# Kernel optimization log

Measured on AMD Instinct MI355X. Metric: run time of the kernel, lower is better.

## Reference

```python
import jax, jax.numpy as jnp
import numpy as np

EMBED_DIM = 512
KERNEL = 17


def setup_inputs() -> dict:
    key = jax.random.key(0)
    ks = jax.random.split(key, 5)
    B, L, C = 2, 8192, EMBED_DIM
    s = C ** -0.5
    x = jax.random.normal(ks[0], (B, L, C), dtype=jnp.float32)
    # weights stored as (in, out); equivalent to torch Linear weight.T
    w_qkv = jax.random.normal(ks[1], (C, 3 * C), dtype=jnp.float32) * s
    w_width = jax.random.normal(ks[2], (C, 1), dtype=jnp.float32) * s
    b_width = jax.random.normal(ks[3], (1,), dtype=jnp.float32) * 0.01
    w_out = jax.random.normal(ks[4], (C, C), dtype=jnp.float32) * s
    return {"x": x, "w_qkv": w_qkv, "w_width": w_width, "b_width": b_width, "w_out": w_out}


def reference(x, w_qkv, w_width, b_width, w_out):
    B, L, C = x.shape
    K = KERNEL
    half_k = K // 2
    scale = C ** -0.5

    qkv = x @ w_qkv                      # [B,L,3C]
    q, k, v = jnp.split(qkv, 3, axis=-1)

    # learned soft window width in [1, K]
    width = jax.nn.sigmoid(x @ w_width + b_width) * (K - 1) + 1.0   # [B,L,1]

    # sliding windows of k/v: pad along L then gather K-sized windows
    k_pad = jnp.pad(k, ((0, 0), (half_k, half_k), (0, 0)))
    v_pad = jnp.pad(v, ((0, 0), (half_k, half_k), (0, 0)))
    idx = jnp.arange(L)[:, None] + jnp.arange(K)[None, :]           # [L,K]
    k_win = k_pad[:, idx]                # [B,L,K,C]
    v_win = v_pad[:, idx]                # [B,L,K,C]

    scores = jnp.einsum('blc,blkc->blk', q, k_win) * scale          # [B,L,K]

    rel_pos = jnp.abs(jnp.arange(K, dtype=jnp.float32) - half_k)    # [K]
    soft_mask = jax.nn.sigmoid((width - rel_pos) * 5.0)             # [B,L,K]
    scores = scores - (1.0 - soft_mask) * 10000.0

    attn = jax.nn.softmax(scores, axis=-1)
    out = jnp.einsum('blk,blkc->blc', attn, v_win)                  # [B,L,C]
    return (out + v) @ w_out
```

## Files before the change

### kernel.cpp

```cpp
#include <hip/hip_runtime.h>

typedef unsigned short u16;
typedef unsigned int   u32;
typedef __attribute__((ext_vector_type(8))) short          shortx8;
typedef __attribute__((ext_vector_type(8))) unsigned short ushortx8;
typedef __attribute__((ext_vector_type(4))) float          floatx4;

#define AS1 __attribute__((address_space(1)))
#define AS3 __attribute__((address_space(3)))

#define SEG 8208
#define LV  16416

__device__ __forceinline__ float b2f(u16 v) {
  return __uint_as_float(((u32)v) << 16);
}
__device__ __forceinline__ u16 f2b(float f) {
  u32 u = __float_as_uint(f);
  u += 0x7FFF + ((u >> 16) & 1);
  return (u16)(u >> 16);
}
__device__ __forceinline__ void cp16(const void* g, void* l) {
  __builtin_amdgcn_global_load_lds((AS1 u32*)g, (AS3 u32*)l, 16, 0, 0);
}

__global__ __launch_bounds__(256)
void prep(const float* __restrict__ x, const float* __restrict__ w_width,
          const float* __restrict__ b_width, const float* __restrict__ w_qkv,
          const float* __restrict__ w_out, u16* __restrict__ xb,
          float* __restrict__ width, u16* __restrict__ BtAll,
          u16* __restrict__ Vt) {
  __shared__ alignas(16) u16 shb[17408];
  const int b = blockIdx.x;
  if (b < 32) {
    const bool isMc = (b < 16);
    const int t    = isMc ? b : b - 16;
    const int row0 = (t >> 2) * 128;
    const int col0 = (t & 3) * 128;
    const int tid  = threadIdx.x;
    const int lane = tid & 63;
    const int wave = tid >> 6;
    const int quad = lane >> 4;
    const int lr   = lane & 15;
    const int wr   = (wave >> 1) * 64;
    const int wc   = (wave & 1) * 64;
    u16* As = shb;
    u16* Bs = shb + 8192;

    floatx4 acc[4][4];
#pragma unroll
    for (int i = 0; i < 4; ++i)
#pragma unroll
      for (int j = 0; j < 4; ++j) acc[i][j] = (floatx4)0.0f;

    int srow[4], scol[4];
#pragma unroll
    for (int p = 0; p < 4; ++p) {
      int c = p * 256 + tid;
      srow[p] = c >> 3;
      scol[p] = ((c & 7) ^ (srow[p] & 7)) * 8;
    }
    const int swz = lr & 7;

    for (int k0 = 0; k0 < 512; k0 += 64) {
#pragma unroll
      for (int p = 0; p < 4; ++p) {
        const float* ga = w_qkv + (size_t)(row0 + srow[p]) * 1536 +
                          (isMc ? 0 : 1024) + k0 + scol[p];
        floatx4 a0 = *(const floatx4*)ga;
        floatx4 a1 = *(const floatx4*)(ga + 4);
        ushortx8 o;
#pragma unroll
        for (int j = 0; j < 4; ++j) { o[j] = f2b(a0[j]); o[4 + j] = f2b(a1[j]); }
        *(ushortx8*)&As[(p * 256 + tid) * 8] = o;
      }
#pragma unroll
      for (int p = 0; p < 4; ++p) {
        ushortx8 o;
        if (isMc) {
          const float* gb = w_qkv + (size_t)(col0 + srow[p]) * 1536 + 512 +
                            k0 + scol[p];
          floatx4 b0 = *(const floatx4*)gb;
          floatx4 b1 = *(const floatx4*)(gb + 4);
#pragma unroll
          for (int j = 0; j < 4; ++j) { o[j] = f2b(b0[j]); o[4 + j] = f2b(b1[j]); }
        } else {
          const float* gb = w_out + (size_t)(k0 + scol[p]) * 512 + col0 + srow[p];
#pragma unroll
          for (int j = 0; j < 8; ++j) o[j] = f2b(gb[(size_t)j * 512]);
        }
        *(ushortx8*)&Bs[(p * 256 + tid) * 8] = o;
      }
      __syncthreads();
#pragma unroll
      for (int ks = 0; ks < 2; ++ks) {
        shortx8 af[4], bf[4];
#pragma unroll
        for (int mi = 0; mi < 4; ++mi)
          af[mi] = *(const shortx8*)
              &As[((wr + mi * 16 + lr) * 8 + ((ks * 4 + quad) ^ swz)) * 8];
#pragma unroll
        for (int ni = 0; ni < 4; ++ni)
          bf[ni] = *(const shortx8*)
              &Bs[((wc + ni * 16 + lr) * 8 + ((ks * 4 + quad) ^ swz)) * 8];
#pragma unroll
        for (int mi = 0; mi < 4; ++mi)
#pragma unroll
          for (int ni = 0; ni < 4; ++ni)
            acc[mi][ni] = __builtin_amdgcn_mfma_f32_16x16x32_bf16(
                af[mi], bf[ni], acc[mi][ni], 0, 0, 0);
      }
      __syncthreads();
    }
    u16* outp = BtAll + (isMc ? 0 : (size_t)512 * 512);
#pragma unroll
    for (int mi = 0; mi < 4; ++mi)
#pragma unroll
      for (int ni = 0; ni < 4; ++ni)
#pragma unroll
        for (int r = 0; r < 4; ++r)
          shb[(wc + ni * 16 + lr) * 136 + wr + mi * 16 + quad * 4 + r] =
              f2b(acc[mi][ni][r]);
    __syncthreads();
    const int rr = tid >> 4, cc = (tid & 15) * 8;
#pragma unroll
    for (int it = 0; it < 8; ++it) {
      int chl = it * 16 + rr;
      *(ushortx8*)(outp + (size_t)(col0 + chl) * 512 + row0 + cc) =
          *(const ushortx8*)&shb[chl * 136 + cc];
    }
  } else if (b < 4128) {
    const int lane = threadIdx.x & 63;
    const int row  = (b - 32) * 4 + (threadIdx.x >> 6);
    const float* xp = x + (size_t)row * 512 + lane * 8;
    floatx4 v0 = *(const floatx4*)xp;
    floatx4 v1 = *(const floatx4*)(xp + 4);
    floatx4 w0 = *(const floatx4*)(w_width + lane * 8);
    floatx4 w1 = *(const floatx4*)(w_width + lane * 8 + 4);
    float s = 0.f;
    ushortx8 o;
#pragma unroll
    for (int j = 0; j < 4; ++j) {
      s += v0[j] * w0[j] + v1[j] * w1[j];
      o[j] = f2b(v0[j]); o[4 + j] = f2b(v1[j]);
    }
    *(ushortx8*)(xb + (size_t)row * 512 + lane * 8) = o;
#pragma unroll
    for (int m = 32; m >= 1; m >>= 1) s += __shfl_xor(s, m, 64);
    if (lane == 0)
      width[row] = 16.f / (1.f + __expf(-(s + b_width[0]))) + 1.f;
  } else {
    const int idx = (b - 4128) * 256 + threadIdx.x;
    const int ch = idx >> 5;
    const int k  = idx & 31;
    const int seg = k >> 4;
    const int j   = k & 15;
    const int col = seg * SEG + (j < 8 ? j : 8192 + j);
    Vt[(size_t)ch * LV + col] = 0;
  }
}

__global__ __launch_bounds__(256, 3)
void gemm_qv(const u16* __restrict__ A, const u16* __restrict__ Bt,
             u16* __restrict__ Qb, u16* __restrict__ Vt) {
  const int K = 512;
  __shared__ alignas(16) u16 lds[17408];
  u16* As = lds;
  u16* Bs = lds + 8192;
  const int tid  = threadIdx.x;
  const int lane = tid & 63;
  const int wave = tid >> 6;
  const int quad = lane >> 4;
  const int lr   = lane & 15;
  const int row0 = blockIdx.x * 128;
  const int col0 = blockIdx.y * 128;
  const int wr   = (wave >> 1) * 64;
  const int wc   = (wave & 1) * 64;

  floatx4 acc[4][4];
#pragma unroll
  for (int i = 0; i < 4; ++i)
#pragma unroll
    for (int j = 0; j < 4; ++j) acc[i][j] = (floatx4)0.0f;

  int srow[4], scol[4];
#pragma unroll
  for (int p = 0; p < 4; ++p) {
    int c = p * 256 + tid;
    srow[p] = c >> 3;
    scol[p] = ((c & 7) ^ (srow[p] & 7)) * 8;
  }
  const int swz = lr & 7;

  for (int k0 = 0; k0 < K; k0 += 64) {
#pragma unroll
    for (int p = 0; p < 4; ++p)
      cp16(A + (size_t)(row0 + srow[p]) * K + k0 + scol[p], &As[(p * 256 + tid) * 8]);
#pragma unroll
    for (int p = 0; p < 4; ++p)
      cp16(Bt + (size_t)(col0 + srow[p]) * K + k0 + scol[p], &Bs[(p * 256 + tid) * 8]);
    __syncthreads();

#pragma unroll
    for (int ks = 0; ks < 2; ++ks) {
      shortx8 af[4], bf[4];
#pragma unroll
      for (int mi = 0; mi < 4; ++mi)
        af[mi] = *(const shortx8*)
            &As[((wr + mi * 16 + lr) * 8 + ((ks * 4 + quad) ^ swz)) * 8];
#pragma unroll
      for (int ni = 0; ni < 4; ++ni)
        bf[ni] = *(const shortx8*)
            &Bs[((wc + ni * 16 + lr) * 8 + ((ks * 4 + quad) ^ swz)) * 8];
#pragma unroll
      for (int mi = 0; mi < 4; ++mi)
#pragma unroll
        for (int ni = 0; ni < 4; ++ni)
          acc[mi][ni] = __builtin_amdgcn_mfma_f32_16x16x32_bf16(
              af[mi], bf[ni], acc[mi][ni], 0, 0, 0);
    }
    __syncthreads();
  }

  if (col0 < 512) {
    const int cb = col0;
#pragma unroll
    for (int mi = 0; mi < 4; ++mi)
#pragma unroll
      for (int ni = 0; ni < 4; ++ni)
#pragma unroll
        for (int r = 0; r < 4; ++r)
          lds[(wr + mi * 16 + quad * 4 + r) * 136 + wc + ni * 16 + lr] =
              f2b(acc[mi][ni][r]);
    __syncthreads();
    const int rr = tid >> 4, cc = (tid & 15) * 8;
#pragma unroll
    for (int it = 0; it < 8; ++it) {
      int row = it * 16 + rr;
      *(ushortx8*)(Qb + (size_t)(row0 + row) * 512 + cb + cc) =
          *(const ushortx8*)&lds[row * 136 + cc];
    }
  } else {
    const int cb = col0 - 512;
    const int bb = row0 >> 13, pib0 = row0 & 8191;
#pragma unroll
    for (int mi = 0; mi < 4; ++mi)
#pragma unroll
      for (int ni = 0; ni < 4; ++ni)
#pragma unroll
        for (int r = 0; r < 4; ++r)
          lds[(wc + ni * 16 + lr) * 136 + wr + mi * 16 + quad * 4 + r] =
              f2b(acc[mi][ni][r]);
    __syncthreads();
    const int rr = tid >> 4, cc = (tid & 15) * 8;
#pragma unroll
    for (int it = 0; it < 8; ++it) {
      int chl = it * 16 + rr;
      ushortx8 v = *(const ushortx8*)&lds[chl * 136 + cc];
      *(ushortx8*)(Vt + (size_t)(cb + chl) * LV + (size_t)bb * SEG + 8 + pib0 + cc) = v;
    }
  }
}

__global__ __launch_bounds__(256, 1)
void attn_fused(const u16* __restrict__ Q, const u16* __restrict__ Kx,
                const u16* __restrict__ Vt, const float* __restrict__ width,
                float* __restrict__ Out) {
  __shared__ alignas(16) u16 P[4][16][32];
  const int tid  = threadIdx.x;
  const int lane = tid & 63;
  const int wave = tid >> 6;
  const int quad = lane >> 4;
  const int lr   = lane & 15;
  const int p0   = blockIdx.x * 64;
  const int pw   = p0 + wave * 16;
  const int pibw = pw & 8191;
  const int bb   = pw >> 13;
  const size_t cb0 = (size_t)bb * SEG + pibw;

  shortx8 vfA[16];
#pragma unroll
  for (int ctl = 0; ctl < 16; ++ctl)
    vfA[ctl] = *(const shortx8*)(Vt + (size_t)(ctl * 16 + lr) * LV +
                                 cb0 + quad * 8);

  floatx4 s0 = (floatx4)0.0f, s1 = (floatx4)0.0f;
#pragma unroll 4
  for (int s = 0; s < 16; ++s) {
    const int k0 = s * 32 + quad * 8;
    shortx8 af = *(const shortx8*)(Q  + (size_t)(pw + lr) * 512 + k0);
    shortx8 f0 = *(const shortx8*)(Kx + (ptrdiff_t)(pw - 8 + lr) * 512 + k0);
    shortx8 f1 = *(const shortx8*)(Kx + (ptrdiff_t)(pw + 8 + lr) * 512 + k0);
    s0 = __builtin_amdgcn_mfma_f32_16x16x32_bf16(af, f0, s0, 0, 0, 0);
    s1 = __builtin_amdgcn_mfma_f32_16x16x32_bf16(af, f1, s1, 0, 0, 0);
  }

  shortx8 vfB[16];
#pragma unroll
  for (int ctl = 0; ctl < 16; ++ctl)
    vfB[ctl] = *(const shortx8*)(Vt + (size_t)(256 + ctl * 16 + lr) * LV +
                                 cb0 + quad * 8);

  {
    const float scale = 0.044194173824159216f;
    floatx4 wv = *(const floatx4*)(width + pw + quad * 4);
#pragma unroll
    for (int r = 0; r < 4; ++r) {
      const int row = quad * 4 + r;
      const int d0  = lr - row;
      const int d1  = d0 + 16;
      const int jb0 = pibw + lr - 8;
      const int jb1 = jb0 + 16;
      float rel0 = fabsf((float)(d0 - 8));
      float rel1 = fabsf((float)(d1 - 8));
      float mk0 = 1.f / (1.f + __expf(-5.f * (wv[r] - rel0)));
      float mk1 = 1.f / (1.f + __expf(-5.f * (wv[r] - rel1)));
      float val0 = (d0 >= 0)
          ? (((unsigned)jb0 < 8192u ? s0[r] * scale : 0.f) - (1.f - mk0) * 10000.f)
          : -1e30f;
      float val1 = (d1 <= 16)
          ? (((unsigned)jb1 < 8192u ? s1[r] * scale : 0.f) - (1.f - mk1) * 10000.f)
          : -1e30f;
      float mx = fmaxf(val0, val1);
#pragma unroll
      for (int m = 8; m >= 1; m >>= 1) mx = fmaxf(mx, __shfl_xor(mx, m, 64));
      float e0 = __expf(val0 - mx), e1 = __expf(val1 - mx);
      float sum = e0 + e1;
#pragma unroll
      for (int m = 8; m >= 1; m >>= 1) sum += __shfl_xor(sum, m, 64);
      const float inv = 1.f / sum;
      P[wave][row][lr]      = f2b(e0 * inv + (d0 == 8 ? 1.f : 0.f));
      P[wave][row][lr + 16] = f2b(e1 * inv + (d1 == 8 ? 1.f : 0.f));
    }
  }
  shortx8 pf = *(const shortx8*)&P[wave][lr][quad * 8];

#pragma unroll
  for (int ctl = 0; ctl < 16; ++ctl) {
    floatx4 o = __builtin_amdgcn_mfma_f32_16x16x32_bf16(pf, vfA[ctl],
                                                        (floatx4)0.0f, 0, 0, 0);
#pragma unroll
    for (int r = 0; r < 4; ++r)
      Out[(size_t)(pw + quad * 4 + r) * 512 + ctl * 16 + lr] = o[r];
  }
#pragma unroll
  for (int ctl = 0; ctl < 16; ++ctl) {
    floatx4 o = __builtin_amdgcn_mfma_f32_16x16x32_bf16(pf, vfB[ctl],
                                                        (floatx4)0.0f, 0, 0, 0);
#pragma unroll
    for (int r = 0; r < 4; ++r)
      Out[(size_t)(pw + quad * 4 + r) * 512 + 256 + ctl * 16 + lr] = o[r];
  }
}

extern "C" void kernel_launch(void* const* d_in, const int* in_sizes, int n_in,
                              void* d_out, int out_size, void* d_ws, size_t ws_size,
                              hipStream_t stream) {
  const float* x       = (const float*)d_in[0];
  const float* w_qkv   = (const float*)d_in[1];
  const float* w_width = (const float*)d_in[2];
  const float* b_width = (const float*)d_in[3];
  const float* w_out   = (const float*)d_in[4];
  float* out = (float*)d_out;

  const int M = 16384;
  char* ws = (char*)d_ws;
  u16*   xb    = (u16*)(ws + 8192);
  u16*   Qb    = (u16*)(ws + 16793600);
  u16*   Vt    = (u16*)(ws + 33579008);
  u16*   BtAll = (u16*)(ws + 50397184);
  float* width = (float*)(ws + 51445760);

  prep<<<dim3(4192), dim3(256), 0, stream>>>(x, w_width, b_width, w_qkv, w_out,
                                             xb, width, BtAll, Vt);
  gemm_qv<<<dim3(M / 128, 8), dim3(256), 0, stream>>>(xb, BtAll, Qb, Vt);
  attn_fused<<<dim3(M / 64), dim3(256), 0, stream>>>(Qb, xb, Vt, width, out);
}
```

Before: 165.0 us.

## Coalesce w_out loads in prep, remap GEMM and attention blocks for locality

The prep kernel now loads w_out with coalesced float4 row reads and scatters them transposed into the swizzled LDS tile, replacing strided per-element column reads. gemm_qv uses a 1D grid with an XCD-aware block remap so blocks sharing rows land on the same die. attn_fused now splits channels across waves, giving 32 positions per block and twice as many blocks with occupancy 2, plus an XCD-aware block order. The width buffer offset moves. The attention split recomputes the QK scores in two waves per row group, which adds duplicated work.

After: 153.6 us. 6.9% less time.

```diff
diff --git a/kernel.cpp b/kernel.cpp
--- a/kernel.cpp
+++ b/kernel.cpp
@@ -74,22 +74,32 @@
         for (int j = 0; j < 4; ++j) { o[j] = f2b(a0[j]); o[4 + j] = f2b(a1[j]); }
         *(ushortx8*)&As[(p * 256 + tid) * 8] = o;
       }
-#pragma unroll
-      for (int p = 0; p < 4; ++p) {
-        ushortx8 o;
-        if (isMc) {
+      if (isMc) {
+#pragma unroll
+        for (int p = 0; p < 4; ++p) {
           const float* gb = w_qkv + (size_t)(col0 + srow[p]) * 1536 + 512 +
                             k0 + scol[p];
           floatx4 b0 = *(const floatx4*)gb;
           floatx4 b1 = *(const floatx4*)(gb + 4);
+          ushortx8 o;
 #pragma unroll
           for (int j = 0; j < 4; ++j) { o[j] = f2b(b0[j]); o[4 + j] = f2b(b1[j]); }
-        } else {
-          const float* gb = w_out + (size_t)(k0 + scol[p]) * 512 + col0 + srow[p];
-#pragma unroll
-          for (int j = 0; j < 8; ++j) o[j] = f2b(gb[(size_t)j * 512]);
+          *(ushortx8*)&Bs[(p * 256 + tid) * 8] = o;
         }
-        *(ushortx8*)&Bs[(p * 256 + tid) * 8] = o;
+      } else {
+#pragma unroll
+        for (int it = 0; it < 8; ++it) {
+          int e  = it * 1024 + tid * 4;
+          int kk = e >> 7;
+          int j  = e & 127;
+          floatx4 b4 = *(const floatx4*)(w_out + (size_t)(k0 + kk) * 512 +
+                                         col0 + j);
+#pragma unroll
+          for (int q = 0; q < 4; ++q) {
+            int r = j + q;
+            Bs[(r * 8 + ((kk >> 3) ^ (r & 7))) * 8 + (kk & 7)] = f2b(b4[q]);
+          }
+        }
       }
       __syncthreads();
 #pragma unroll
@@ -172,8 +182,9 @@
   const int wave = tid >> 6;
   const int quad = lane >> 4;
   const int lr   = lane & 15;
-  const int row0 = blockIdx.x * 128;
-  const int col0 = blockIdx.y * 128;
+  const int logical = (blockIdx.x & 7) * 128 + (blockIdx.x >> 3);
+  const int row0 = (logical >> 3) * 128;
+  const int col0 = (logical & 7) * 128;
   const int wr   = (wave >> 1) * 64;
   const int wc   = (wave & 1) * 64;
 
@@ -262,7 +273,7 @@
   }
 }
 
-__global__ __launch_bounds__(256, 1)
+__global__ __launch_bounds__(256, 2)
 void attn_fused(const u16* __restrict__ Q, const u16* __restrict__ Kx,
                 const u16* __restrict__ Vt, const float* __restrict__ width,
                 float* __restrict__ Out) {
@@ -272,16 +283,19 @@
   const int wave = tid >> 6;
   const int quad = lane >> 4;
   const int lr   = lane & 15;
-  const int p0   = blockIdx.x * 64;
-  const int pw   = p0 + wave * 16;
+  const int p0   = ((blockIdx.x & 7) * 64 + (blockIdx.x >> 3)) * 32;
+  const int rg   = wave & 1;
+  const int chh  = wave >> 1;
+  const int ch0  = chh * 256;
+  const int pw   = p0 + rg * 16;
   const int pibw = pw & 8191;
   const int bb   = pw >> 13;
   const size_t cb0 = (size_t)bb * SEG + pibw;
 
-  shortx8 vfA[16];
-#pragma unroll
-  for (int ctl = 0; ctl < 16; ++ctl)
-    vfA[ctl] = *(const shortx8*)(Vt + (size_t)(ctl * 16 + lr) * LV +
+  shortx8 vfA[8];
+#pragma unroll
+  for (int ctl = 0; ctl < 8; ++ctl)
+    vfA[ctl] = *(const shortx8*)(Vt + (size_t)(ch0 + ctl * 16 + lr) * LV +
                                  cb0 + quad * 8);
 
   floatx4 s0 = (floatx4)0.0f, s1 = (floatx4)0.0f;
@@ -295,10 +309,10 @@
     s1 = __builtin_amdgcn_mfma_f32_16x16x32_bf16(af, f1, s1, 0, 0, 0);
   }
 
-  shortx8 vfB[16];
-#pragma unroll
-  for (int ctl = 0; ctl < 16; ++ctl)
-    vfB[ctl] = *(const shortx8*)(Vt + (size_t)(256 + ctl * 16 + lr) * LV +
+  shortx8 vfB[8];
+#pragma unroll
+  for (int ctl = 0; ctl < 8; ++ctl)
+    vfB[ctl] = *(const shortx8*)(Vt + (size_t)(ch0 + 128 + ctl * 16 + lr) * LV +
                                  cb0 + quad * 8);
 
   {
@@ -336,20 +350,20 @@
   shortx8 pf = *(const shortx8*)&P[wave][lr][quad * 8];
 
 #pragma unroll
-  for (int ctl = 0; ctl < 16; ++ctl) {
+  for (int ctl = 0; ctl < 8; ++ctl) {
     floatx4 o = __builtin_amdgcn_mfma_f32_16x16x32_bf16(pf, vfA[ctl],
                                                         (floatx4)0.0f, 0, 0, 0);
 #pragma unroll
     for (int r = 0; r < 4; ++r)
-      Out[(size_t)(pw + quad * 4 + r) * 512 + ctl * 16 + lr] = o[r];
-  }
-#pragma unroll
-  for (int ctl = 0; ctl < 16; ++ctl) {
+      Out[(size_t)(pw + quad * 4 + r) * 512 + ch0 + ctl * 16 + lr] = o[r];
+  }
+#pragma unroll
+  for (int ctl = 0; ctl < 8; ++ctl) {
     floatx4 o = __builtin_amdgcn_mfma_f32_16x16x32_bf16(pf, vfB[ctl],
                                                         (floatx4)0.0f, 0, 0, 0);
 #pragma unroll
     for (int r = 0; r < 4; ++r)
-      Out[(size_t)(pw + quad * 4 + r) * 512 + 256 + ctl * 16 + lr] = o[r];
+      Out[(size_t)(pw + quad * 4 + r) * 512 + ch0 + 128 + ctl * 16 + lr] = o[r];
   }
 }
 
@@ -369,10 +383,10 @@
   u16*   Qb    = (u16*)(ws + 16793600);
   u16*   Vt    = (u16*)(ws + 33579008);
   u16*   BtAll = (u16*)(ws + 50397184);
-  float* width = (float*)(ws + 51445760);
-
-  prep<<<dim3(4192), dim3(256), 0, stream>>>(x, w_width, b_width, w_qkv, w_out,
-                                             xb, width, BtAll, Vt);
-  gemm_qv<<<dim3(M / 128, 8), dim3(256), 0, stream>>>(xb, BtAll, Qb, Vt);
-  attn_fused<<<dim3(M / 64), dim3(256), 0, stream>>>(Qb, xb, Vt, width, out);
-}
+  float* width = (float*)(ws + 51970048);
+
+  prep<<<dim3(4192), dim3(256), 0, stream>>>(x, w_width, b_width, w_qkv,
+                                             w_out, xb, width, BtAll, Vt);
+  gemm_qv<<<dim3(1024), dim3(256), 0, stream>>>(xb, BtAll, Qb, Vt);
+  attn_fused<<<dim3(M / 32), dim3(256), 0, stream>>>(Qb, xb, Vt, width, out);
+}
```
